# Kernel tuning notes

Measured on AMD Instinct MI355X. Metric: run time of the kernel, lower is better.

Reference implementation:

```python
import jax, jax.numpy as jnp
import numpy as np


def setup_inputs() -> dict:
    key = jax.random.key(0)
    k1, k2, k3, k4, k5 = jax.random.split(key, 5)
    B, T, R, H = 64, 256, 49, 1024  # batch, caption len, regions (7x7), hidden
    V = jax.random.normal(k1, (B, R, H), dtype=jnp.float32)
    h_t = jax.random.normal(k2, (B, T, H), dtype=jnp.float32)
    Wv = jax.random.normal(k3, (R, H), dtype=jnp.float32) * (1.0 / np.sqrt(H))
    Wg = jax.random.normal(k4, (R, H), dtype=jnp.float32) * (1.0 / np.sqrt(H))
    Wh = jax.random.normal(k5, (1, R), dtype=jnp.float32) * (1.0 / np.sqrt(R))
    return {"V": V, "h_t": h_t, "Wv": Wv, "Wg": Wg, "Wh": Wh}


def reference(V, h_t, Wv, Wg, Wh):
    # content_v: [B,1,R,R] + [B,T,1,R] -> [B,T,R,R]
    cv = jnp.einsum('brh,kh->brk', V, Wv)      # [B, R, R]
    cg = jnp.einsum('bth,kh->btk', h_t, Wg)    # [B, T, R]
    content_v = cv[:, None, :, :] + cg[:, :, None, :]  # [B, T, R, R]
    # z_t = affine_h(tanh(content_v)) squeezed -> [B, T, R]
    z_t = jnp.einsum('btrk,k->btr', jnp.tanh(content_v), Wh[0])
    alpha_t = jax.nn.softmax(z_t, axis=-1)     # [B, T, R]
    c_t = jnp.einsum('btr,brh->bth', alpha_t, V)  # [B, T, H]
    return (c_t, alpha_t)
```

## Files before the change

kernel.cpp:

```cpp
#include <hip/hip_runtime.h>
#include <hip/hip_bf16.h>
#include <math.h>
#include <stdint.h>


typedef __attribute__((ext_vector_type(8))) short bf16x8;
typedef __attribute__((ext_vector_type(4))) float floatx4;

static __device__ __forceinline__ bf16x8 pack8(float4 a, float4 b) {
    union { __hip_bfloat162 h[4]; bf16x8 v; } u;
    u.h[0] = __float22bfloat162_rn(make_float2(a.x, a.y));
    u.h[1] = __float22bfloat162_rn(make_float2(a.z, a.w));
    u.h[2] = __float22bfloat162_rn(make_float2(b.x, b.y));
    u.h[3] = __float22bfloat162_rn(make_float2(b.z, b.w));
    return u.v;
}

static __device__ __forceinline__ unsigned short f2bf_bits(float f) {
    union { __hip_bfloat16 h; unsigned short u; } c;
    c.h = __float2bfloat16(f);
    return c.u;
}

__global__ __launch_bounds__(256) void gemm_mfma_tr(const float* __restrict__ Av,
                                                    const float* __restrict__ Ag,
                                                    const float* __restrict__ Wv,
                                                    const float* __restrict__ Wg,
                                                    float* __restrict__ Cv,
                                                    float* __restrict__ Cg,
                                                    unsigned short* __restrict__ vT) {
    __shared__ __align__(16) char smem[49 * 132 * 4];
    const int bid = blockIdx.x;
    const int tid = threadIdx.x;

    if (bid >= 610) {
        float* Ts = (float*)smem;
        const int tb = bid - 610;
        const int b = tb >> 3;
        const int h0 = (tb & 7) * 128;
        for (int i = tid; i < 49 * 32; i += 256) {
            const int r = i >> 5, hq = i & 31;
            *(float4*)(Ts + r * 132 + hq * 4) =
                *(const float4*)(Av + ((size_t)b * 49 + r) * 1024 + h0 + hq * 4);
        }
        __syncthreads();
        const int h = tid & 127;
        const int half = tid >> 7;
        float f[32];
#pragma unroll
        for (int j = 0; j < 32; ++j) {
            const int r = half * 32 + j;
            f[j] = (r < 49) ? Ts[r * 132 + h] : 0.f;
        }
        const size_t rowbase = ((size_t)b * 1024 + h0 + h) * 64;
#pragma unroll
        for (int o2 = 0; o2 < 4; ++o2) {
            const int o = half * 4 + o2;
            bf16x8 v = pack8(make_float4(f[o2*8+0], f[o2*8+1], f[o2*8+2], f[o2*8+3]),
                             make_float4(f[o2*8+4], f[o2*8+5], f[o2*8+6], f[o2*8+7]));
            *(bf16x8*)(vT + rowbase + (size_t)((o ^ (h & 7)) * 8)) = v;
        }
        return;
    }

    short* As = (short*)smem;
    short* Ws = (short*)(smem + 4096);
    const float* A; const float* W; float* C; int m0;
    if (bid < 98) { A = Av; W = Wv; C = Cv; m0 = bid * 32; }
    else          { A = Ag; W = Wg; C = Cg; m0 = (bid - 98) * 32; }

    const int wave = tid >> 6, lane = tid & 63;
    const int quad = lane >> 4, l16 = lane & 15;
    const int mb = (wave & 1) * 16;
    const int nb = (wave >> 1) * 32;

    floatx4 acc[2] = {};

    const int arow = tid >> 3, ag = tid & 7;
    const int wrow = tid >> 2, wq = tid & 3;
    const float* aptr = A + (size_t)(m0 + arow) * 1024 + ag * 8;
    const bool wvalid = wrow < 49;
    const float* wptr = W + (size_t)wrow * 1024 + wq * 16;

    float4 a0 = *(const float4*)(aptr);
    float4 a1 = *(const float4*)(aptr + 4);
    float4 w0 = make_float4(0.f,0.f,0.f,0.f), w1 = w0, w2 = w0, w3 = w0;
    if (wvalid) {
        w0 = *(const float4*)(wptr);
        w1 = *(const float4*)(wptr + 4);
        w2 = *(const float4*)(wptr + 8);
        w3 = *(const float4*)(wptr + 12);
    }

    for (int kc = 0; kc < 1024; kc += 64) {
        __syncthreads();
        *(bf16x8*)(As + arow * 64 + (ag ^ (arow & 7)) * 8) = pack8(a0, a1);
        *(bf16x8*)(Ws + wrow * 64 + ((wq * 2) ^ (wrow & 7)) * 8) = pack8(w0, w1);
        *(bf16x8*)(Ws + wrow * 64 + ((wq * 2 + 1) ^ (wrow & 7)) * 8) = pack8(w2, w3);
        __syncthreads();
        if (kc < 960) {
            a0 = *(const float4*)(aptr + kc + 64);
            a1 = *(const float4*)(aptr + kc + 68);
            if (wvalid) {
                w0 = *(const float4*)(wptr + kc + 64);
                w1 = *(const float4*)(wptr + kc + 68);
                w2 = *(const float4*)(wptr + kc + 72);
                w3 = *(const float4*)(wptr + kc + 76);
            }
        }
#pragma unroll
        for (int s = 0; s < 2; ++s) {
            const int am = mb + l16;
            bf16x8 af = *(const bf16x8*)(As + am * 64 + (((s << 2) + quad) ^ (am & 7)) * 8);
#pragma unroll
            for (int nt = 0; nt < 2; ++nt) {
                const int wn = nb + nt * 16 + l16;
                bf16x8 bf = *(const bf16x8*)(Ws + wn * 64 + (((s << 2) + quad) ^ (wn & 7)) * 8);
                acc[nt] = __builtin_amdgcn_mfma_f32_16x16x32_bf16(af, bf, acc[nt], 0, 0, 0);
            }
        }
    }

#pragma unroll
    for (int nt = 0; nt < 2; ++nt) {
        const int n = nb + nt * 16 + l16;
        if (n < 49) {
#pragma unroll
            for (int r = 0; r < 4; ++r) {
                const int m = m0 + mb + quad * 4 + r;
                C[(size_t)m * 49 + n] = acc[nt][r];
            }
        }
    }
}

__global__ __launch_bounds__(256) void zsoftmax_ct(const float* __restrict__ cv,
                                                   const float* __restrict__ cg,
                                                   const float* __restrict__ Wh,
                                                   const unsigned short* __restrict__ vT,
                                                   float* __restrict__ alpha,
                                                   float* __restrict__ C) {
    const int b = blockIdx.x >> 3;
    const int t0 = (blockIdx.x & 7) * 32;

    __shared__ __align__(16) char smem[4096 + 49 * 52 * 4 + 32 * 52 * 4 + 52 * 4];
    short* Al  = (short*)smem;
    float* cvl = (float*)(smem + 4096);
    float* cgl = cvl + 49 * 52;
    float* whl = cgl + 32 * 52;
    short* Vl  = (short*)(smem + 4096);

    const int tid = threadIdx.x;
    for (int i = tid; i < 49 * 49; i += 256) {
        int r = i / 49, k = i - r * 49;
        cvl[r * 52 + k] = cv[(size_t)b * 2401 + i];
    }
    for (int i = tid; i < 32 * 49; i += 256) {
        int t = i / 49, k = i - t * 49;
        cgl[t * 52 + k] = cg[((size_t)b * 256 + t0) * 49 + i];
    }
    if (tid < 52) whl[tid] = (tid < 49) ? Wh[tid] : 0.f;
    __syncthreads();

    const int wave = tid >> 6;
    const int lane = tid & 63;
    const int quad = lane >> 4, l16 = lane & 15;
    const float4* cvr = (const float4*)(cvl + lane * 52);
    const float4* wh4 = (const float4*)whl;

    for (int i = 0; i < 8; ++i) {
        const int tl = wave * 8 + i;
        float z = -INFINITY;
        if (lane < 49) {
            const float4* cgr = (const float4*)(cgl + tl * 52);
            float s = 0.f;
#pragma unroll 4
            for (int kk = 0; kk < 12; ++kk) {
                float4 x = cvr[kk], g = cgr[kk], w = wh4[kk];
                float r0 = __builtin_amdgcn_rcpf(__expf(2.f * (x.x + g.x)) + 1.f);
                float r1 = __builtin_amdgcn_rcpf(__expf(2.f * (x.y + g.y)) + 1.f);
                float r2 = __builtin_amdgcn_rcpf(__expf(2.f * (x.z + g.z)) + 1.f);
                float r3 = __builtin_amdgcn_rcpf(__expf(2.f * (x.w + g.w)) + 1.f);
                s = fmaf(1.f - 2.f * r0, w.x, s);
                s = fmaf(1.f - 2.f * r1, w.y, s);
                s = fmaf(1.f - 2.f * r2, w.z, s);
                s = fmaf(1.f - 2.f * r3, w.w, s);
            }
            {
                float x = cvl[lane * 52 + 48] + cgl[tl * 52 + 48];
                float r0 = __builtin_amdgcn_rcpf(__expf(2.f * x) + 1.f);
                s = fmaf(1.f - 2.f * r0, whl[48], s);
            }
            z = s;
        }
        float m = z;
        for (int off = 32; off; off >>= 1) m = fmaxf(m, __shfl_xor(m, off));
        float p = (lane < 49) ? __expf(z - m) : 0.f;
        float sum = p;
        for (int off = 32; off; off >>= 1) sum += __shfl_xor(sum, off);
        const float val = p * __builtin_amdgcn_rcpf(sum);

        const size_t grow = (size_t)b * 256 + t0 + tl;
        if (lane < 49) alpha[grow * 49 + lane] = val;
        const int pos = (((lane >> 3) ^ (tl & 7)) << 3) | (lane & 7);
        Al[tl * 64 + pos] = (short)f2bf_bits(val);
    }
    __syncthreads();

    const int tb = (wave & 1) * 16;
    const int hb = (wave >> 1) * 64;

    bf16x8 af[2];
    {
        const int row = tb + l16;
#pragma unroll
        for (int kc = 0; kc < 2; ++kc)
            af[kc] = *(const bf16x8*)(Al + row * 64 + (((kc << 2) + quad) ^ (row & 7)) * 8);
    }

    const bf16x8* vsrc = (const bf16x8*)(vT + ((size_t)b * 1024) * 64);
    bf16x8 vreg[4];
#pragma unroll
    for (int p = 0; p < 4; ++p) vreg[p] = vsrc[tid + p * 256];

    for (int c = 0; c < 8; ++c) {
        bf16x8* dst = (bf16x8*)Vl;
#pragma unroll
        for (int p = 0; p < 4; ++p) dst[tid + p * 256] = vreg[p];
        __syncthreads();
        if (c < 7) {
#pragma unroll
            for (int p = 0; p < 4; ++p) vreg[p] = vsrc[(size_t)(c + 1) * 1024 + tid + p * 256];
        }

        floatx4 acc[4] = {};
#pragma unroll
        for (int kc = 0; kc < 2; ++kc) {
#pragma unroll
            for (int ns = 0; ns < 4; ++ns) {
                const int row = hb + ns * 16 + l16;
                bf16x8 bf = *(const bf16x8*)(Vl + row * 64 + (((kc << 2) + quad) ^ (row & 7)) * 8);
                acc[ns] = __builtin_amdgcn_mfma_f32_16x16x32_bf16(af[kc], bf, acc[ns], 0, 0, 0);
            }
        }

        const int h0 = c << 7;
#pragma unroll
        for (int ns = 0; ns < 4; ++ns) {
            const int h = h0 + hb + ns * 16 + l16;
#pragma unroll
            for (int r = 0; r < 4; ++r) {
                const int tg = t0 + tb + quad * 4 + r;
                C[((size_t)b * 256 + tg) * 1024 + h] = acc[ns][r];
            }
        }
        __syncthreads();
    }
}

extern "C" void kernel_launch(void* const* d_in, const int* in_sizes, int n_in,
                              void* d_out, int out_size, void* d_ws, size_t ws_size,
                              hipStream_t stream) {
    const float* V   = (const float*)d_in[0];
    const float* h_t = (const float*)d_in[1];
    const float* Wv  = (const float*)d_in[2];
    const float* Wg  = (const float*)d_in[3];
    const float* Wh  = (const float*)d_in[4];

    float* c_t   = (float*)d_out;
    float* alpha = (float*)d_out + 16777216;

    float* cv = (float*)d_ws;
    float* cg = cv + 153664;
    unsigned short* vT = (unsigned short*)((char*)d_ws + 3825920);

    gemm_mfma_tr<<<610 + 512, 256, 0, stream>>>(V, h_t, Wv, Wg, cv, cg, vT);
    zsoftmax_ct<<<512, 256, 0, stream>>>(cv, cg, Wh, vT, alpha, c_t);
}
```

Before: 182.0 us.

## Halve per-block time tile, read V fragments directly from global, remap blocks

The fused softmax/context kernel now handles 16 caption positions per block instead of 32, which doubles the grid to 1024 blocks. Each wave reads its bf16 V fragments straight from global memory (through cache) instead of staging them in shared memory behind barriers, and computes 256 hidden columns in one pass with 16 accumulators. The block index is also remapped so that neighbouring blocks fall on different batches. The aim is more parallelism and fewer syncs and LDS copies, at the cost of reloading cv and V per block, more register pressure, and possibly less coalesced global loads.

```diff
diff --git a/kernel.cpp b/kernel.cpp
--- a/kernel.cpp
+++ b/kernel.cpp
@@ -140,22 +140,22 @@
                                                    const unsigned short* __restrict__ vT,
                                                    float* __restrict__ alpha,
                                                    float* __restrict__ C) {
-    const int b = blockIdx.x >> 3;
-    const int t0 = (blockIdx.x & 7) * 32;
-
-    __shared__ __align__(16) char smem[4096 + 49 * 52 * 4 + 32 * 52 * 4 + 52 * 4];
-    short* Al  = (short*)smem;
-    float* cvl = (float*)(smem + 4096);
-    float* cgl = cvl + 49 * 52;
-    float* whl = cgl + 32 * 52;
-    short* Vl  = (short*)(smem + 4096);
+    const int bid = blockIdx.x;
+    const int orig = (bid & 7) * 128 + (bid >> 3);
+    const int b = orig >> 4;
+    const int t0 = (orig & 15) * 16;
+
+    __shared__ __align__(16) short Al[16 * 64];
+    __shared__ __align__(16) float cvl[49 * 52];
+    __shared__ __align__(16) float cgl[16 * 52];
+    __shared__ __align__(16) float whl[52];
 
     const int tid = threadIdx.x;
     for (int i = tid; i < 49 * 49; i += 256) {
         int r = i / 49, k = i - r * 49;
         cvl[r * 52 + k] = cv[(size_t)b * 2401 + i];
     }
-    for (int i = tid; i < 32 * 49; i += 256) {
+    for (int i = tid; i < 16 * 49; i += 256) {
         int t = i / 49, k = i - t * 49;
         cgl[t * 52 + k] = cg[((size_t)b * 256 + t0) * 49 + i];
     }
@@ -168,8 +168,9 @@
     const float4* cvr = (const float4*)(cvl + lane * 52);
     const float4* wh4 = (const float4*)whl;
 
-    for (int i = 0; i < 8; ++i) {
-        const int tl = wave * 8 + i;
+#pragma unroll
+    for (int i = 0; i < 4; ++i) {
+        const int tl = wave * 4 + i;
         float z = -INFINITY;
         if (lane < 49) {
             const float4* cgr = (const float4*)(cgl + tl * 52);
@@ -207,54 +208,33 @@
     }
     __syncthreads();
 
-    const int tb = (wave & 1) * 16;
-    const int hb = (wave >> 1) * 64;
-
     bf16x8 af[2];
-    {
-        const int row = tb + l16;
-#pragma unroll
-        for (int kc = 0; kc < 2; ++kc)
-            af[kc] = *(const bf16x8*)(Al + row * 64 + (((kc << 2) + quad) ^ (row & 7)) * 8);
-    }
-
-    const bf16x8* vsrc = (const bf16x8*)(vT + ((size_t)b * 1024) * 64);
-    bf16x8 vreg[4];
-#pragma unroll
-    for (int p = 0; p < 4; ++p) vreg[p] = vsrc[tid + p * 256];
-
-    for (int c = 0; c < 8; ++c) {
-        bf16x8* dst = (bf16x8*)Vl;
-#pragma unroll
-        for (int p = 0; p < 4; ++p) dst[tid + p * 256] = vreg[p];
-        __syncthreads();
-        if (c < 7) {
-#pragma unroll
-            for (int p = 0; p < 4; ++p) vreg[p] = vsrc[(size_t)(c + 1) * 1024 + tid + p * 256];
-        }
-
-        floatx4 acc[4] = {};
-#pragma unroll
-        for (int kc = 0; kc < 2; ++kc) {
-#pragma unroll
-            for (int ns = 0; ns < 4; ++ns) {
-                const int row = hb + ns * 16 + l16;
-                bf16x8 bf = *(const bf16x8*)(Vl + row * 64 + (((kc << 2) + quad) ^ (row & 7)) * 8);
-                acc[ns] = __builtin_amdgcn_mfma_f32_16x16x32_bf16(af[kc], bf, acc[ns], 0, 0, 0);
-            }
-        }
-
-        const int h0 = c << 7;
-#pragma unroll
-        for (int ns = 0; ns < 4; ++ns) {
-            const int h = h0 + hb + ns * 16 + l16;
-#pragma unroll
-            for (int r = 0; r < 4; ++r) {
-                const int tg = t0 + tb + quad * 4 + r;
-                C[((size_t)b * 256 + tg) * 1024 + h] = acc[ns][r];
-            }
-        }
-        __syncthreads();
+#pragma unroll
+    for (int kc = 0; kc < 2; ++kc)
+        af[kc] = *(const bf16x8*)(Al + l16 * 64 + (((kc << 2) + quad) ^ (l16 & 7)) * 8);
+
+    const int hb = wave * 256;
+    const unsigned short* vb = vT + ((size_t)b * 1024 + hb) * 64;
+
+    floatx4 acc[16] = {};
+#pragma unroll
+    for (int ns = 0; ns < 16; ++ns) {
+        const int row = ns * 16 + l16;
+        const unsigned short* vrow = vb + (size_t)row * 64;
+        bf16x8 b0 = *(const bf16x8*)(vrow + ((quad ^ (row & 7)) * 8));
+        bf16x8 b1 = *(const bf16x8*)(vrow + (((4 + quad) ^ (row & 7)) * 8));
+        acc[ns] = __builtin_amdgcn_mfma_f32_16x16x32_bf16(af[0], b0, acc[ns], 0, 0, 0);
+        acc[ns] = __builtin_amdgcn_mfma_f32_16x16x32_bf16(af[1], b1, acc[ns], 0, 0, 0);
+    }
+
+#pragma unroll
+    for (int ns = 0; ns < 16; ++ns) {
+        const int h = hb + ns * 16 + l16;
+#pragma unroll
+        for (int r = 0; r < 4; ++r) {
+            const int t = t0 + quad * 4 + r;
+            C[((size_t)b * 256 + t) * 1024 + h] = acc[ns][r];
+        }
     }
 }
 
@@ -275,5 +255,5 @@
     unsigned short* vT = (unsigned short*)((char*)d_ws + 3825920);
 
     gemm_mfma_tr<<<610 + 512, 256, 0, stream>>>(V, h_t, Wv, Wg, cv, cg, vT);
-    zsoftmax_ct<<<512, 256, 0, stream>>>(cv, cg, Wh, vT, alpha, c_t);
-}
+    zsoftmax_ct<<<1024, 256, 0, stream>>>(cv, cg, Wh, vT, alpha, c_t);
+}
```

Result: faster. 174.0 us (-4.4%).
